# Optimization experiments

Hardware: AMD Instinct MI355X
Metric: run time of the kernel (lower is better)

Reference implementation:

```python
import jax, jax.numpy as jnp
import numpy as np

B = 8           # hardcoded batchsize in the original forward
EPS = 1e-4      # scn.BatchNormalization default eps


def setup_inputs() -> dict:
    key = jax.random.key(0)
    ks = jax.random.split(key, 8)
    Nq, Nkv = 16384, 32768
    dec_in, enc_in, nf = 64, 64, 128
    nbr = jax.random.randint(ks[2], (Nq, 27), 0, Nq, dtype=jnp.int32)
    # center tap of the 3x3x3 submanifold conv is the point itself
    nbr = nbr.at[:, 13].set(jnp.arange(Nq, dtype=jnp.int32))
    return {
        "x_decoder_feat": jax.random.normal(ks[0], (Nq, dec_in), jnp.float32),
        "x_encoder_feat": jax.random.normal(ks[1], (Nkv, enc_in), jnp.float32),
        "nbr_idx": nbr,
        "W_p1": jax.random.normal(ks[3], (27, dec_in, nf), jnp.float32) * 0.05,
        "W_q": jax.random.normal(ks[4], (nf, nf), jnp.float32) * 0.05,
        "W_k": jax.random.normal(ks[5], (enc_in, nf), jnp.float32) * 0.05,
        "W_v": jax.random.normal(ks[6], (enc_in, nf), jnp.float32) * 0.05,
        "W_trans": jax.random.normal(ks[7], (nf, nf), jnp.float32) * 0.05,
        "gamma": jnp.ones((nf,), jnp.float32),
        "beta": jnp.zeros((nf,), jnp.float32),
    }


def reference(x_decoder_feat, x_encoder_feat, nbr_idx, W_p1, W_q, W_k, W_v,
              W_trans, gamma, beta):
    nf = W_q.shape[1]
    # p1: 3x3x3 submanifold conv = gather 27 neighbors, per-offset matmul, sum
    x_dec = jnp.einsum('nkc,kcf->nf', x_decoder_feat[nbr_idx], W_p1)  # [Nq,nf]
    q = (x_dec @ W_q).reshape(B, -1, nf)            # [B, nq, nf]
    k = (x_encoder_feat @ W_k).reshape(B, -1, nf)   # [B, nkv, nf]
    v = (x_encoder_feat @ W_v).reshape(B, -1, nf)
    # per-batch QK^T softmax V (no 1/sqrt(d) scaling in original)
    attn = jax.nn.softmax(jnp.einsum('bqc,bkc->bqk', q, k), axis=-1)
    x_r = jnp.einsum('bqk,bkc->bqc', attn, v).reshape(-1, nf)  # [Nq,nf]
    # trans_conv (1x1) + batchnorm (batch stats over all points)
    t = x_r @ W_trans
    mean = t.mean(axis=0)
    var = t.var(axis=0)
    bn = (t - mean) * jax.lax.rsqrt(var + EPS) * gamma + beta
    return x_dec + bn
```

## Files before the change

### kernel.cpp

```cpp
#include <hip/hip_runtime.h>
#include <math.h>

#define NQ      16384
#define NKV     32768
#define CIN     64
#define NF      128
#define NOFF    27
#define BATCH   8
#define SQ      2048
#define SKV     4096
#define BN_EPS  1e-4f
#define SPLIT   4
#define KV_PER_SPLIT (SKV / SPLIT)
#define TILES_PER_SPLIT (KV_PER_SPLIT / 64)
#define LOG2E   1.4426950408889634f
#define SHIFT2  57.70780163555854f

typedef unsigned short u16;
typedef __attribute__((ext_vector_type(4))) float f32x4;
typedef __attribute__((ext_vector_type(8))) short s16x8;

__device__ __forceinline__ u16 f2b(float x) {
    union { float f; unsigned u; } c; c.f = x;
    unsigned r = (c.u + 0x7FFFu + ((c.u >> 16) & 1u)) >> 16;
    return (u16)r;
}
__device__ __forceinline__ float b2f(u16 x) {
    union { unsigned u; float f; } c; c.u = ((unsigned)x) << 16;
    return c.f;
}
__device__ __forceinline__ void g2l16(const void* gp, void* lp) {
    __builtin_amdgcn_global_load_lds(
        (const __attribute__((address_space(1))) unsigned*)gp,
        (__attribute__((address_space(3))) unsigned*)lp, 16, 0, 0);
}

__device__ __forceinline__ void wtrans_one(
    const float* __restrict__ src, u16* __restrict__ dst, int K, int id, float sc)
{
    int n  = id / (K / 4);
    int k4 = (id % (K / 4)) * 4;
    const float* s = src + (size_t)k4 * NF + n;
    ushort4 o;
    o.x = f2b(s[0] * sc); o.y = f2b(s[NF] * sc);
    o.z = f2b(s[2 * NF] * sc); o.w = f2b(s[3 * NF] * sc);
    *(ushort4*)(dst + (size_t)n * K + k4) = o;
}

__global__ __launch_bounds__(256) void prep_kernel(
    const float* __restrict__ xdec_feat, const float* __restrict__ Wp1,
    const float* __restrict__ Wq, const float* __restrict__ Wk,
    const float* __restrict__ Wv, const float* __restrict__ Wt,
    u16* __restrict__ xf_bf, u16* __restrict__ wp1t,
    u16* __restrict__ wqT, u16* __restrict__ wkT,
    u16* __restrict__ wvT, u16* __restrict__ wtT,
    float* __restrict__ stats)
{
    int bid = blockIdx.x;
    int t   = threadIdx.x;
    if (bid < 1024) {
        int i = (bid * 256 + t) * 4;
        float4 v = *(const float4*)(xdec_feat + i);
        ushort4 o;
        o.x = f2b(v.x); o.y = f2b(v.y); o.z = f2b(v.z); o.w = f2b(v.w);
        *(ushort4*)(xf_bf + i) = o;
    } else if (bid < 1240) {
        int id = (bid - 1024) * 256 + t;
        int ko = id >> 11;
        int r  = id & 2047;
        int f  = r >> 4;
        int c4 = (r & 15) * 4;
        const float* s = Wp1 + (size_t)ko * 8192 + (size_t)c4 * NF + f;
        ushort4 o;
        o.x = f2b(s[0]); o.y = f2b(s[NF]); o.z = f2b(s[2 * NF]); o.w = f2b(s[3 * NF]);
        *(ushort4*)(wp1t + (size_t)ko * 8192 + (size_t)f * 64 + c4) = o;
    } else if (bid < 1288) {
        int id = (bid - 1240) * 256 + t;
        if (id < 4096)        wtrans_one(Wq, wqT, 128, id, LOG2E);
        else if (id < 6144)   wtrans_one(Wk, wkT, 64, id - 4096, 1.f);
        else if (id < 8192)   wtrans_one(Wv, wvT, 64, id - 6144, 1.f);
        else                  wtrans_one(Wt, wtT, 128, id - 8192, 1.f);
    } else {
        stats[t] = 0.f;
    }
}

__global__ __launch_bounds__(256) void main_fused_kernel(
    const float* __restrict__ xenc, const u16* __restrict__ xf,
    const int* __restrict__ nbr, const u16* __restrict__ wp1t,
    const u16* __restrict__ wqT, const u16* __restrict__ wkT,
    const u16* __restrict__ wvT,
    u16* __restrict__ kbuf, u16* __restrict__ vt,
    float* __restrict__ xdec, u16* __restrict__ qbuf)
{
    __shared__ u16 Bs[2][128][64];
    __shared__ int nbr_s[64][28];

    const int t    = threadIdx.x;
    const int w    = t >> 6;
    const int lane = t & 63;
    const int quad = lane >> 4;
    const int l15  = lane & 15;

    if (blockIdx.x < 512) {
        const int m0 = blockIdx.x * 64 + w * 16;
        const float* Ap = xenc + (size_t)(m0 + l15) * CIN + quad * 8;
        float4 a0 = *(const float4*)(Ap);
        float4 a1 = *(const float4*)(Ap + 4);
        float4 a2 = *(const float4*)(Ap + 32);
        float4 a3 = *(const float4*)(Ap + 36);
        union { u16 a[8]; s16x8 v; } p0, p1;
        p0.a[0] = f2b(a0.x); p0.a[1] = f2b(a0.y); p0.a[2] = f2b(a0.z); p0.a[3] = f2b(a0.w);
        p0.a[4] = f2b(a1.x); p0.a[5] = f2b(a1.y); p0.a[6] = f2b(a1.z); p0.a[7] = f2b(a1.w);
        p1.a[0] = f2b(a2.x); p1.a[1] = f2b(a2.y); p1.a[2] = f2b(a2.z); p1.a[3] = f2b(a2.w);
        p1.a[4] = f2b(a3.x); p1.a[5] = f2b(a3.y); p1.a[6] = f2b(a3.z); p1.a[7] = f2b(a3.w);
        s16x8 af0 = p0.v, af1 = p1.v;

        int m  = m0 + quad * 4;
        int bb = m >> 12;
        int kv = m & 4095;
        #pragma unroll
        for (int nt = 0; nt < 8; nt++) {
            f32x4 ka = (f32x4)0.f, va = (f32x4)0.f;
            const u16* Kp = wkT + (size_t)(nt * 16 + l15) * CIN + quad * 8;
            const u16* Vp = wvT + (size_t)(nt * 16 + l15) * CIN + quad * 8;
            s16x8 kb0 = *(const s16x8*)(Kp);
            s16x8 kb1 = *(const s16x8*)(Kp + 32);
            s16x8 vb0 = *(const s16x8*)(Vp);
            s16x8 vb1 = *(const s16x8*)(Vp + 32);
            ka = __builtin_amdgcn_mfma_f32_16x16x32_bf16(af0, kb0, ka, 0, 0, 0);
            ka = __builtin_amdgcn_mfma_f32_16x16x32_bf16(af1, kb1, ka, 0, 0, 0);
            va = __builtin_amdgcn_mfma_f32_16x16x32_bf16(af0, vb0, va, 0, 0, 0);
            va = __builtin_amdgcn_mfma_f32_16x16x32_bf16(af1, vb1, va, 0, 0, 0);
            #pragma unroll
            for (int r = 0; r < 4; r++)
                kbuf[(size_t)(m0 + quad * 4 + r) * NF + nt * 16 + l15] = f2b(ka[r]);
            ushort4 pk;
            pk.x = f2b(va[0]); pk.y = f2b(va[1]); pk.z = f2b(va[2]); pk.w = f2b(va[3]);
            *(ushort4*)(vt + (size_t)(bb * NF + nt * 16 + l15) * SKV + kv) = pk;
        }
        return;
    }

    const int base = (blockIdx.x - 512) * 64;

    for (int i = t; i < 64 * NOFF; i += 256)
        nbr_s[i / NOFF][i % NOFF] = nbr[(size_t)base * NOFF + i];

    f32x4 oacc[8];
    #pragma unroll
    for (int n = 0; n < 8; n++) oacc[n] = (f32x4)0.f;

    const int arow = w * 16 + l15;
    const int sr   = w * 32 + (lane >> 3);

    #pragma unroll
    for (int c = 0; c < 4; c++) {
        int row = sr + c * 8;
        int kk  = (lane & 7) ^ (row & 7);
        g2l16(wp1t + (size_t)row * 64 + kk * 8, &Bs[0][w * 32 + c * 8][0]);
    }
    __syncthreads();

    for (int ko = 0; ko < NOFF; ko++) {
        int cur = ko & 1;
        if (ko + 1 < NOFF) {
            int nxt = (ko + 1) & 1;
            #pragma unroll
            for (int c = 0; c < 4; c++) {
                int row = sr + c * 8;
                int kk  = (lane & 7) ^ (row & 7);
                g2l16(wp1t + (size_t)(ko + 1) * 8192 + (size_t)row * 64 + kk * 8,
                      &Bs[nxt][w * 32 + c * 8][0]);
            }
        }
        int nb = nbr_s[arow][ko];
        const u16* ap = xf + (size_t)nb * CIN + quad * 8;
        s16x8 af0 = *(const s16x8*)(ap);
        s16x8 af1 = *(const s16x8*)(ap + 32);
        #pragma unroll
        for (int nt = 0; nt < 8; nt++) {
            int pc0 = quad ^ (l15 & 7);
            int pc1 = (4 + quad) ^ (l15 & 7);
            s16x8 bf0 = *(const s16x8*)&Bs[cur][nt * 16 + l15][pc0 * 8];
            s16x8 bf1 = *(const s16x8*)&Bs[cur][nt * 16 + l15][pc1 * 8];
            oacc[nt] = __builtin_amdgcn_mfma_f32_16x16x32_bf16(af0, bf0, oacc[nt], 0, 0, 0);
            oacc[nt] = __builtin_amdgcn_mfma_f32_16x16x32_bf16(af1, bf1, oacc[nt], 0, 0, 0);
        }
        __syncthreads();
    }

    u16* xq = &Bs[0][0][0];
    #pragma unroll
    for (int nt = 0; nt < 8; nt++)
        #pragma unroll
        for (int r = 0; r < 4; r++) {
            int row = w * 16 + quad * 4 + r;
            int col = nt * 16 + l15;
            xdec[(size_t)(base + row) * NF + col] = oacc[nt][r];
            xq[row * 136 + col] = f2b(oacc[nt][r]);
        }

    s16x8 aq[4];
    #pragma unroll
    for (int ks = 0; ks < 4; ks++)
        aq[ks] = *(const s16x8*)&xq[(w * 16 + l15) * 136 + ks * 32 + quad * 8];

    #pragma unroll
    for (int nt = 0; nt < 8; nt++) {
        f32x4 acc = (f32x4)0.f;
        const u16* Wp = wqT + (size_t)(nt * 16 + l15) * NF + quad * 8;
        #pragma unroll
        for (int ks = 0; ks < 4; ks++) {
            s16x8 bf = *(const s16x8*)(Wp + ks * 32);
            acc = __builtin_amdgcn_mfma_f32_16x16x32_bf16(aq[ks], bf, acc, 0, 0, 0);
        }
        #pragma unroll
        for (int r = 0; r < 4; r++)
            qbuf[(size_t)(base + w * 16 + quad * 4 + r) * NF + nt * 16 + l15] = f2b(acc[r]);
    }
}

__global__ __launch_bounds__(256) void attn_mfma_kernel(
    const u16* __restrict__ Q, const u16* __restrict__ K,
    const u16* __restrict__ Vt, u16* __restrict__ Opart,
    float* __restrict__ lpart)
{
    __shared__ u16 Ks[64][128];
    __shared__ u16 Vs[128][64];
    __shared__ u16 Ps[4][32][72];

    const int t    = threadIdx.x;
    const int b    = blockIdx.y;
    const int q0   = blockIdx.x * 128;
    const int sp   = blockIdx.z;
    const int w    = t >> 6;
    const int lane = t & 63;
    const int quad = lane >> 4;
    const int l15  = lane & 15;

    const u16* Kb  = K  + (size_t)b * SKV * NF;
    const u16* Vtb = Vt + (size_t)b * NF * SKV;

    s16x8 qf[2][4];
    #pragma unroll
    for (int g = 0; g < 2; g++) {
        const u16* Qp = Q + ((size_t)(b * SQ + q0 + w * 32 + g * 16 + l15)) * NF + quad * 8;
        #pragma unroll
        for (int ks = 0; ks < 4; ks++) qf[g][ks] = *(const s16x8*)(Qp + ks * 32);
    }

    f32x4 oacc[2][8];
    #pragma unroll
    for (int g = 0; g < 2; g++)
        #pragma unroll
        for (int n = 0; n < 8; n++) oacc[g][n] = (f32x4)0.f;
    float lrow[2] = {0.f, 0.f};

    const int kvbase = sp * KV_PER_SPLIT;

    for (int tile = 0; tile < TILES_PER_SPLIT; tile++) {
        int kv0 = kvbase + tile * 64;
        __syncthreads();
        #pragma unroll
        for (int c = 0; c < 4; c++) {
            int row = w * 16 + c * 4 + (lane >> 4);
            int k8  = (lane & 15) ^ (row & 15);
            g2l16(Kb + (size_t)(kv0 + row) * NF + k8 * 8, &Ks[w * 16 + c * 4][0]);
        }
        #pragma unroll
        for (int c = 0; c < 4; c++) {
            int row = w * 32 + c * 8 + (lane >> 3);
            int k8  = (lane & 7) ^ (row & 7);
            g2l16(Vtb + (size_t)row * SKV + kv0 + k8 * 8, &Vs[w * 32 + c * 8][0]);
        }
        __syncthreads();

        f32x4 sacc[2][4];
        #pragma unroll
        for (int c = 0; c < 4; c++) {
            sacc[0][c] = (f32x4)0.f;
            sacc[1][c] = (f32x4)0.f;
            #pragma unroll
            for (int ks = 0; ks < 4; ks++) {
                int p = (ks * 4 + quad) ^ l15;
                s16x8 ka = *(const s16x8*)&Ks[c * 16 + l15][p * 8];
                sacc[0][c] = __builtin_amdgcn_mfma_f32_16x16x32_bf16(ka, qf[0][ks], sacc[0][c], 0, 0, 0);
                sacc[1][c] = __builtin_amdgcn_mfma_f32_16x16x32_bf16(ka, qf[1][ks], sacc[1][c], 0, 0, 0);
            }
        }

        #pragma unroll
        for (int g = 0; g < 2; g++) {
            float rs = 0.f;
            float pv[4][4];
            #pragma unroll
            for (int c = 0; c < 4; c++)
                #pragma unroll
                for (int r = 0; r < 4; r++) {
                    float p = exp2f(sacc[g][c][r] - SHIFT2);
                    pv[c][r] = p;
                    rs += p;
                }
            rs += __shfl_xor(rs, 16);
            rs += __shfl_xor(rs, 32);
            lrow[g] += rs;
            #pragma unroll
            for (int c = 0; c < 4; c++) {
                ushort4 pk;
                pk.x = f2b(pv[c][0]); pk.y = f2b(pv[c][1]);
                pk.z = f2b(pv[c][2]); pk.w = f2b(pv[c][3]);
                *(ushort4*)&Ps[w][g * 16 + l15][c * 16 + quad * 4] = pk;
            }
        }

        s16x8 pb[2][2];
        #pragma unroll
        for (int g = 0; g < 2; g++) {
            pb[g][0] = *(const s16x8*)&Ps[w][g * 16 + l15][quad * 8];
            pb[g][1] = *(const s16x8*)&Ps[w][g * 16 + l15][32 + quad * 8];
        }
        #pragma unroll
        for (int mt = 0; mt < 8; mt++) {
            int p0 = quad ^ (l15 & 7);
            int p1 = (4 + quad) ^ (l15 & 7);
            s16x8 va0 = *(const s16x8*)&Vs[mt * 16 + l15][p0 * 8];
            s16x8 va1 = *(const s16x8*)&Vs[mt * 16 + l15][p1 * 8];
            oacc[0][mt] = __builtin_amdgcn_mfma_f32_16x16x32_bf16(va0, pb[0][0], oacc[0][mt], 0, 0, 0);
            oacc[0][mt] = __builtin_amdgcn_mfma_f32_16x16x32_bf16(va1, pb[0][1], oacc[0][mt], 0, 0, 0);
            oacc[1][mt] = __builtin_amdgcn_mfma_f32_16x16x32_bf16(va0, pb[1][0], oacc[1][mt], 0, 0, 0);
            oacc[1][mt] = __builtin_amdgcn_mfma_f32_16x16x32_bf16(va1, pb[1][1], oacc[1][mt], 0, 0, 0);
        }
    }

    #pragma unroll
    for (int g = 0; g < 2; g++) {
        int grow = b * SQ + q0 + w * 32 + g * 16 + l15;
        u16* Ob = Opart + (size_t)sp * NQ * NF + (size_t)grow * NF;
        #pragma unroll
        for (int mt = 0; mt < 8; mt++) {
            ushort4 ov;
            ov.x = f2b(oacc[g][mt][0]); ov.y = f2b(oacc[g][mt][1]);
            ov.z = f2b(oacc[g][mt][2]); ov.w = f2b(oacc[g][mt][3]);
            *(ushort4*)(Ob + mt * 16 + quad * 4) = ov;
        }
        if (quad == 0) lpart[sp * NQ + grow] = lrow[g];
    }
}

__global__ __launch_bounds__(256) void tgemm_fused_kernel(
    const u16* __restrict__ Opart, const float* __restrict__ lpart,
    const u16* __restrict__ WT, float* __restrict__ C, float* __restrict__ stats)
{
    const int t    = threadIdx.x;
    const int w    = t >> 6;
    const int lane = t & 63;
    const int quad = lane >> 4;
    const int l15  = lane & 15;
    const int m0   = blockIdx.x * 64 + w * 16;
    const int row  = m0 + l15;

    float L = 0.f;
    #pragma unroll
    for (int s = 0; s < SPLIT; s++) L += lpart[s * NQ + row];
    float invL = 1.f / L;

    s16x8 af[4];
    #pragma unroll
    for (int ks = 0; ks < 4; ks++) {
        float sum[8] = {0.f, 0.f, 0.f, 0.f, 0.f, 0.f, 0.f, 0.f};
        #pragma unroll
        for (int s = 0; s < SPLIT; s++) {
            const u16* p = Opart + (size_t)s * NQ * NF + (size_t)row * NF + ks * 32 + quad * 8;
            ushort4 u0 = *(const ushort4*)p;
            ushort4 u1 = *(const ushort4*)(p + 4);
            sum[0] += b2f(u0.x); sum[1] += b2f(u0.y);
            sum[2] += b2f(u0.z); sum[3] += b2f(u0.w);
            sum[4] += b2f(u1.x); sum[5] += b2f(u1.y);
            sum[6] += b2f(u1.z); sum[7] += b2f(u1.w);
        }
        union { u16 a[8]; s16x8 v; } pk;
        #pragma unroll
        for (int j = 0; j < 8; j++) pk.a[j] = f2b(sum[j] * invL);
        af[ks] = pk.v;
    }

    f32x4 oacc[8];
    #pragma unroll
    for (int nt = 0; nt < 8; nt++) {
        oacc[nt] = (f32x4)0.f;
        const u16* Wp = WT + (size_t)(nt * 16 + l15) * NF + quad * 8;
        #pragma unroll
        for (int ks = 0; ks < 4; ks++) {
            s16x8 bf = *(const s16x8*)(Wp + ks * 32);
            oacc[nt] = __builtin_amdgcn_mfma_f32_16x16x32_bf16(af[ks], bf, oacc[nt], 0, 0, 0);
        }
    }

    float s[8], sq[8];
    #pragma unroll
    for (int nt = 0; nt < 8; nt++) {
        s[nt] = 0.f; sq[nt] = 0.f;
        #pragma unroll
        for (int r = 0; r < 4; r++) {
            float v = oacc[nt][r];
            C[(size_t)(m0 + quad * 4 + r) * NF + nt * 16 + l15] = v;
            s[nt] += v; sq[nt] += v * v;
        }
    }
    #pragma unroll
    for (int nt = 0; nt < 8; nt++) {
        s[nt]  += __shfl_xor(s[nt], 16);  s[nt]  += __shfl_xor(s[nt], 32);
        sq[nt] += __shfl_xor(sq[nt], 16); sq[nt] += __shfl_xor(sq[nt], 32);
    }
    __shared__ float red[2][4][128];
    if (quad == 0) {
        #pragma unroll
        for (int nt = 0; nt < 8; nt++) {
            red[0][w][nt * 16 + l15] = s[nt];
            red[1][w][nt * 16 + l15] = sq[nt];
        }
    }
    __syncthreads();
    if (t < 128) {
        float a = red[0][0][t] + red[0][1][t] + red[0][2][t] + red[0][3][t];
        atomicAdd(&stats[t], a);
    } else if (t < 256) {
        int f = t - 128;
        float a = red[1][0][f] + red[1][1][f] + red[1][2][f] + red[1][3][f];
        atomicAdd(&stats[128 + f], a);
    }
}

__global__ __launch_bounds__(256) void bn_finalize(
    const float* __restrict__ tbuf, const float* __restrict__ xdec,
    const float* __restrict__ stats, const float* __restrict__ gamma,
    const float* __restrict__ beta, float* __restrict__ out)
{
    const int g = blockIdx.x * 256 + threadIdx.x;
    const int e = g * 4;
    const int f = e & (NF - 1);
    const float invN = 1.0f / (float)NQ;
    float4 tv = *(const float4*)(tbuf + e);
    float4 xv = *(const float4*)(xdec + e);
    float o[4], tt[4] = {tv.x, tv.y, tv.z, tv.w}, xx[4] = {xv.x, xv.y, xv.z, xv.w};
    #pragma unroll
    for (int u = 0; u < 4; u++) {
        float sum  = stats[f + u];
        float sumq = stats[128 + f + u];
        float mean = sum * invN;
        float var  = sumq * invN - mean * mean;
        float sc   = rsqrtf(var + BN_EPS) * gamma[f + u];
        o[u] = xx[u] + (tt[u] - mean) * sc + beta[f + u];
    }
    float4 ov = make_float4(o[0], o[1], o[2], o[3]);
    *(float4*)(out + e) = ov;
}

extern "C" void kernel_launch(void* const* d_in, const int* in_sizes, int n_in,
                              void* d_out, int out_size, void* d_ws, size_t ws_size,
                              hipStream_t stream) {
    const float* xdec_feat = (const float*)d_in[0];
    const float* xenc_feat = (const float*)d_in[1];
    const int*   nbr       = (const int*)d_in[2];
    const float* Wp1       = (const float*)d_in[3];
    const float* Wq        = (const float*)d_in[4];
    const float* Wk        = (const float*)d_in[5];
    const float* Wv        = (const float*)d_in[6];
    const float* Wt        = (const float*)d_in[7];
    const float* gamma     = (const float*)d_in[8];
    const float* beta      = (const float*)d_in[9];
    float* out = (float*)d_out;

    char* wsb = (char*)d_ws;
    const size_t MB = 1024 * 1024;
    float* xdec   = (float*)(wsb + 0);
    u16*   qbuf   = (u16*)  (wsb + 8 * MB);
    u16*   kbuf   = (u16*)  (wsb + 12 * MB);
    u16*   vt     = (u16*)  (wsb + 20 * MB);
    u16*   opart  = (u16*)  (wsb + 28 * MB);
    u16*   xf_bf  = (u16*)  (wsb + 44 * MB);
    u16*   wp1t   = (u16*)  (wsb + 46 * MB);
    u16*   wqT    = (u16*)  (wsb + 46 * MB + 512 * 1024);
    u16*   wkT    = (u16*)  (wsb + 46 * MB + 512 * 1024 + 32768);
    u16*   wvT    = (u16*)  (wsb + 46 * MB + 512 * 1024 + 49152);
    u16*   wtT    = (u16*)  (wsb + 46 * MB + 512 * 1024 + 65536);
    float* lpart  = (float*)(wsb + 47 * MB);
    float* stats  = (float*)(wsb + 47 * MB + 512 * 1024);
    float* tbuf   = (float*)(wsb + 12 * MB);

    prep_kernel<<<1289, 256, 0, stream>>>(
        xdec_feat, Wp1, Wq, Wk, Wv, Wt,
        xf_bf, wp1t, wqT, wkT, wvT, wtT, stats);
    main_fused_kernel<<<768, 256, 0, stream>>>(
        xenc_feat, xf_bf, nbr, wp1t, wqT, wkT, wvT,
        kbuf, vt, xdec, qbuf);
    attn_mfma_kernel<<<dim3(SQ / 128, BATCH, SPLIT), 256, 0, stream>>>(
        qbuf, kbuf, vt, opart, lpart);
    tgemm_fused_kernel<<<NQ / 64, 256, 0, stream>>>(opart, lpart, wtT, tbuf, stats);
    bn_finalize<<<(NQ * NF) / 1024, 256, 0, stream>>>(tbuf, xdec, stats, gamma, beta, out);
}
```

Measured before the change: 200.4 us.

## Double-buffer K/V tiles in attention kernel and use cheaper bf16 packing

The attention kernel now keeps two LDS buffers for the K and V tiles. It prefetches the next tile with global_load_lds while the MFMAs run on the current tile, and one barrier per iteration replaces two. The P staging buffer shrinks to one 16-row slab per wave that both query groups reuse. Float-to-bf16 conversion now uses a perm-based two-value pack with round-half-up instead of round-to-nearest-even. The aim is to hide global load latency and cut conversion ALU work, at the cost of more LDS (which may lower occupancy) and a small rounding difference.

```diff
diff --git a/kernel.cpp b/kernel.cpp
--- a/kernel.cpp
+++ b/kernel.cpp
@@ -17,6 +17,7 @@
 #define SHIFT2  57.70780163555854f
 
 typedef unsigned short u16;
+typedef unsigned int   u32;
 typedef __attribute__((ext_vector_type(4))) float f32x4;
 typedef __attribute__((ext_vector_type(8))) short s16x8;
 
@@ -28,6 +29,11 @@
 __device__ __forceinline__ float b2f(u16 x) {
     union { unsigned u; float f; } c; c.u = ((unsigned)x) << 16;
     return c.f;
+}
+__device__ __forceinline__ u32 pk2bf(float lo, float hi) {
+    union { float f; u32 u; } a, b;
+    a.f = lo; b.f = hi;
+    return __builtin_amdgcn_perm(b.u + 0x8000u, a.u + 0x8000u, 0x07060302u);
 }
 __device__ __forceinline__ void g2l16(const void* gp, void* lp) {
     __builtin_amdgcn_global_load_lds(
@@ -226,9 +232,9 @@
     const u16* __restrict__ Vt, u16* __restrict__ Opart,
     float* __restrict__ lpart)
 {
-    __shared__ u16 Ks[64][128];
-    __shared__ u16 Vs[128][64];
-    __shared__ u16 Ps[4][32][72];
+    __shared__ u16 Ks[2][64][128];
+    __shared__ u16 Vs[2][128][64];
+    __shared__ u16 Ps[4][16][72];
 
     const int t    = threadIdx.x;
     const int b    = blockIdx.y;
@@ -258,23 +264,41 @@
     float lrow[2] = {0.f, 0.f};
 
     const int kvbase = sp * KV_PER_SPLIT;
+    const int krow = w * 16 + (lane >> 4);
+    const int vrow = w * 32 + (lane >> 3);
+
+    #pragma unroll
+    for (int c = 0; c < 4; c++) {
+        int row = krow + c * 4;
+        int k8  = (lane & 15) ^ (row & 15);
+        g2l16(Kb + (size_t)(kvbase + row) * NF + k8 * 8, &Ks[0][w * 16 + c * 4][0]);
+    }
+    #pragma unroll
+    for (int c = 0; c < 4; c++) {
+        int row = vrow + c * 8;
+        int k8  = (lane & 7) ^ (row & 7);
+        g2l16(Vtb + (size_t)row * SKV + kvbase + k8 * 8, &Vs[0][w * 32 + c * 8][0]);
+    }
 
     for (int tile = 0; tile < TILES_PER_SPLIT; tile++) {
-        int kv0 = kvbase + tile * 64;
+        const int cur = tile & 1;
         __syncthreads();
-        #pragma unroll
-        for (int c = 0; c < 4; c++) {
-            int row = w * 16 + c * 4 + (lane >> 4);
-            int k8  = (lane & 15) ^ (row & 15);
-            g2l16(Kb + (size_t)(kv0 + row) * NF + k8 * 8, &Ks[w * 16 + c * 4][0]);
-        }
-        #pragma unroll
-        for (int c = 0; c < 4; c++) {
-            int row = w * 32 + c * 8 + (lane >> 3);
-            int k8  = (lane & 7) ^ (row & 7);
-            g2l16(Vtb + (size_t)row * SKV + kv0 + k8 * 8, &Vs[w * 32 + c * 8][0]);
-        }
-        __syncthreads();
+        if (tile + 1 < TILES_PER_SPLIT) {
+            const int nxt = (tile + 1) & 1;
+            int kvn = kvbase + (tile + 1) * 64;
+            #pragma unroll
+            for (int c = 0; c < 4; c++) {
+                int row = krow + c * 4;
+                int k8  = (lane & 15) ^ (row & 15);
+                g2l16(Kb + (size_t)(kvn + row) * NF + k8 * 8, &Ks[nxt][w * 16 + c * 4][0]);
+            }
+            #pragma unroll
+            for (int c = 0; c < 4; c++) {
+                int row = vrow + c * 8;
+                int k8  = (lane & 7) ^ (row & 7);
+                g2l16(Vtb + (size_t)row * SKV + kvn + k8 * 8, &Vs[nxt][w * 32 + c * 8][0]);
+            }
+        }
 
         f32x4 sacc[2][4];
         #pragma unroll
@@ -284,12 +308,13 @@
             #pragma unroll
             for (int ks = 0; ks < 4; ks++) {
                 int p = (ks * 4 + quad) ^ l15;
-                s16x8 ka = *(const s16x8*)&Ks[c * 16 + l15][p * 8];
+                s16x8 ka = *(const s16x8*)&Ks[cur][c * 16 + l15][p * 8];
                 sacc[0][c] = __builtin_amdgcn_mfma_f32_16x16x32_bf16(ka, qf[0][ks], sacc[0][c], 0, 0, 0);
                 sacc[1][c] = __builtin_amdgcn_mfma_f32_16x16x32_bf16(ka, qf[1][ks], sacc[1][c], 0, 0, 0);
             }
         }
 
+        s16x8 pb[2][2];
         #pragma unroll
         for (int g = 0; g < 2; g++) {
             float rs = 0.f;
@@ -307,25 +332,21 @@
             lrow[g] += rs;
             #pragma unroll
             for (int c = 0; c < 4; c++) {
-                ushort4 pk;
-                pk.x = f2b(pv[c][0]); pk.y = f2b(pv[c][1]);
-                pk.z = f2b(pv[c][2]); pk.w = f2b(pv[c][3]);
-                *(ushort4*)&Ps[w][g * 16 + l15][c * 16 + quad * 4] = pk;
+                uint2 pk;
+                pk.x = pk2bf(pv[c][0], pv[c][1]);
+                pk.y = pk2bf(pv[c][2], pv[c][3]);
+                *(uint2*)&Ps[w][l15][c * 16 + quad * 4] = pk;
             }
-        }
-
-        s16x8 pb[2][2];
-        #pragma unroll
-        for (int g = 0; g < 2; g++) {
-            pb[g][0] = *(const s16x8*)&Ps[w][g * 16 + l15][quad * 8];
-            pb[g][1] = *(const s16x8*)&Ps[w][g * 16 + l15][32 + quad * 8];
-        }
+            pb[g][0] = *(const s16x8*)&Ps[w][l15][quad * 8];
+            pb[g][1] = *(const s16x8*)&Ps[w][l15][32 + quad * 8];
+        }
+
         #pragma unroll
         for (int mt = 0; mt < 8; mt++) {
             int p0 = quad ^ (l15 & 7);
             int p1 = (4 + quad) ^ (l15 & 7);
-            s16x8 va0 = *(const s16x8*)&Vs[mt * 16 + l15][p0 * 8];
-            s16x8 va1 = *(const s16x8*)&Vs[mt * 16 + l15][p1 * 8];
+            s16x8 va0 = *(const s16x8*)&Vs[cur][mt * 16 + l15][p0 * 8];
+            s16x8 va1 = *(const s16x8*)&Vs[cur][mt * 16 + l15][p1 * 8];
             oacc[0][mt] = __builtin_amdgcn_mfma_f32_16x16x32_bf16(va0, pb[0][0], oacc[0][mt], 0, 0, 0);
             oacc[0][mt] = __builtin_amdgcn_mfma_f32_16x16x32_bf16(va1, pb[0][1], oacc[0][mt], 0, 0, 0);
             oacc[1][mt] = __builtin_amdgcn_mfma_f32_16x16x32_bf16(va0, pb[1][0], oacc[1][mt], 0, 0, 0);
@@ -339,10 +360,10 @@
         u16* Ob = Opart + (size_t)sp * NQ * NF + (size_t)grow * NF;
         #pragma unroll
         for (int mt = 0; mt < 8; mt++) {
-            ushort4 ov;
-            ov.x = f2b(oacc[g][mt][0]); ov.y = f2b(oacc[g][mt][1]);
-            ov.z = f2b(oacc[g][mt][2]); ov.w = f2b(oacc[g][mt][3]);
-            *(ushort4*)(Ob + mt * 16 + quad * 4) = ov;
+            uint2 ov;
+            ov.x = pk2bf(oacc[g][mt][0], oacc[g][mt][1]);
+            ov.y = pk2bf(oacc[g][mt][2], oacc[g][mt][3]);
+            *(uint2*)(Ob + mt * 16 + quad * 4) = ov;
         }
         if (quad == 0) lpart[sp * NQ + grow] = lrow[g];
     }
```

Result: faster. 194.6 us (-2.9%).
